# Performance work log

Measured on AMD Instinct MI355X. Metric: run time of the kernel, lower is better.

The kernel has to match this reference:

```python
import jax, jax.numpy as jnp
import numpy as np
from jax import lax


def _conv2d(x, w, b, pad):
    out = lax.conv_general_dilated(x, w, window_strides=(1, 1),
                                   padding=[(pad, pad), (pad, pad)])
    return out + b[None, :, None, None]


def _modulated_deform_conv(x, off_w, off_b, w, b, k, pad):
    """Modulated deformable conv (deformable_groups=1, stride=1, 'same' pad)."""
    B, C, H, W = x.shape
    K2 = k * k
    # offset/mask conv: 3*K2 channels -> (dy, dx, mask_logits)
    om = _conv2d(x, off_w, off_b, pad)              # [B, 3*K2, H, W]
    dy, dx, mlog = om[:, :K2], om[:, K2:2 * K2], om[:, 2 * K2:]
    mask = jax.nn.sigmoid(mlog)                     # [B, K2, H, W]

    xp = jnp.pad(x, ((0, 0), (0, 0), (pad, pad), (pad, pad)))
    Hp, Wp = H + 2 * pad, W + 2 * pad
    Ho, Wo = H, W                                   # stride 1, pad = k//2

    ky, kx = jnp.meshgrid(jnp.arange(k), jnp.arange(k), indexing='ij')
    ky = ky.reshape(1, K2, 1, 1).astype(x.dtype)
    kx = kx.reshape(1, K2, 1, 1).astype(x.dtype)
    iy = jnp.arange(Ho, dtype=x.dtype).reshape(1, 1, Ho, 1)
    ix = jnp.arange(Wo, dtype=x.dtype).reshape(1, 1, 1, Wo)

    py = iy + ky + dy                               # [B, K2, Ho, Wo] sample y (padded coords)
    px = ix + kx + dx                               # [B, K2, Ho, Wo] sample x

    y0f = jnp.floor(py); x0f = jnp.floor(px)
    ty = py - y0f; tx = px - x0f
    y0 = y0f.astype(jnp.int32); x0 = x0f.astype(jnp.int32)
    y1 = y0 + 1; x1 = x0 + 1

    xp_flat = xp.reshape(B, C, Hp * Wp)

    def gather(yi, xi):
        valid = ((yi >= 0) & (yi < Hp) & (xi >= 0) & (xi < Wp)).astype(x.dtype)
        yc = jnp.clip(yi, 0, Hp - 1)
        xc = jnp.clip(xi, 0, Wp - 1)
        idx = (yc * Wp + xc).reshape(B, 1, K2 * Ho * Wo)
        v = jnp.take_along_axis(xp_flat, idx, axis=2).reshape(B, C, K2, Ho, Wo)
        return v * valid[:, None]                   # zero-pad outside

    w00 = ((1 - ty) * (1 - tx))[:, None]
    w01 = ((1 - ty) * tx)[:, None]
    w10 = (ty * (1 - tx))[:, None]
    w11 = (ty * tx)[:, None]

    cols = (gather(y0, x0) * w00 + gather(y0, x1) * w01 +
            gather(y1, x0) * w10 + gather(y1, x1) * w11)
    cols = cols * mask[:, None]                     # [B, C, K2, Ho, Wo]

    O = w.shape[0]
    out = jnp.einsum('bckhw,ock->bohw', cols, w.reshape(O, C, K2))
    return out + b[None, :, None, None]


def setup_inputs() -> dict:
    key = jax.random.key(0)
    ks = jax.random.split(key, 12)
    B, Cin, H, W = 8, 64, 56, 56
    Ch = 128  # out_channels // 2

    def rn(k, shape, scale):
        return jax.random.normal(k, shape, dtype=jnp.float32) * scale

    return {
        'x': rn(ks[0], (B, Cin, H, W), 1.0),
        'w3': rn(ks[1], (Ch, Cin, 3, 3), 0.05),
        'b3': rn(ks[2], (Ch,), 0.05),
        'off3_w': rn(ks[3], (3 * 9, Cin, 3, 3), 0.01),
        'off3_b': rn(ks[4], (3 * 9,), 0.01),
        'w5': rn(ks[5], (Ch, Cin, 5, 5), 0.03),
        'b5': rn(ks[6], (Ch,), 0.05),
        'off5_w': rn(ks[7], (3 * 25, Cin, 5, 5), 0.01),
        'off5_b': rn(ks[8], (3 * 25,), 0.01),
        'sub_w': rn(ks[9], (Ch, Cin, 1, 1), 0.1),
        'sub_b': rn(ks[10], (Ch,), 0.05),
    }


def reference(x, w3, b3, off3_w, off3_b, w5, b5, off5_w, off5_b, sub_w, sub_b):
    x3 = _modulated_deform_conv(x, off3_w, off3_b, w3, b3, k=3, pad=1)
    x5 = _modulated_deform_conv(x, off5_w, off5_b, w5, b5, k=5, pad=2)
    xs = _conv2d(x, sub_w, sub_b, pad=0)            # 1x1 shortcut projection
    x3 = x3 + xs
    x5 = x5 + xs
    out = jnp.concatenate((x3, x5), axis=1)
    return jax.nn.relu(out)
```

## Files before the change

kernel.cpp:

```cpp
#include <hip/hip_runtime.h>
#include <hip/hip_bf16.h>
#include <math.h>

typedef __attribute__((ext_vector_type(8))) short short8;
typedef __attribute__((ext_vector_type(4))) float f32x4;

#define US_XP    0
#define N_XP     (8*60*60*64)
#define US_WOFF  (US_XP + N_XP)
#define N_WOFF   (26*2*8*64*8)
#define US_W5    (US_WOFF + N_WOFF)
#define N_W5     (26*2*8*64*8)
#define US_W3    (US_W5 + N_W5)
#define N_W3     (10*2*8*64*8)
#define US_TOT   (US_W3 + N_W3)
#define FB_BYTES (((US_TOT*2) + 15) & ~15)
#define F_BOM    0
#define F_B5     128
#define F_B3     256
#define N_ITEMS  (8*34*3136)
#define F_OFFS   384
#define F_WTS    (F_OFFS + N_ITEMS*4)

__device__ __forceinline__ unsigned short f2bf(float f) {
    union { float f; unsigned u; } v; v.f = f;
    unsigned r = v.u + 0x7FFFu + ((v.u >> 16) & 1u);
    return (unsigned short)(r >> 16);
}
__device__ __forceinline__ unsigned pack2(float lo, float hi) {
    __hip_bfloat162 h = __float22bfloat162_rn(make_float2(lo, hi));
    return *(unsigned*)&h;
}
__device__ __forceinline__ unsigned blend2(unsigned a, unsigned b, unsigned c, unsigned d,
                                           float w00, float w01, float w10, float w11) {
    float lo = __uint_as_float(a << 16) * w00 + __uint_as_float(b << 16) * w01
             + __uint_as_float(c << 16) * w10 + __uint_as_float(d << 16) * w11;
    float hi = __uint_as_float(a & 0xffff0000u) * w00 + __uint_as_float(b & 0xffff0000u) * w01
             + __uint_as_float(c & 0xffff0000u) * w10 + __uint_as_float(d & 0xffff0000u) * w11;
    return pack2(lo, hi);
}

__global__ __launch_bounds__(256) void xpose(const float* __restrict__ x,
                                             unsigned short* __restrict__ xp)
{
    __shared__ float ld[64*65];
    const int b   = blockIdx.y;
    const int px0 = blockIdx.x * 64;
    const int t   = threadIdx.x;
#pragma unroll
    for (int c0 = 0; c0 < 64; c0 += 4) {
        const int c = c0 + (t >> 6);
        const int p = t & 63;
        ld[c*65 + p] = x[((size_t)(b*64 + c))*3136 + px0 + p];
    }
    __syncthreads();
    const int lp = t >> 2;
    const int ch0 = (t & 3) * 16;
    const int px = px0 + lp;
    const int oy = px/56, ox = px - oy*56;
    unsigned short* dst = xp + ((size_t)b*3600 + (oy+2)*60 + (ox+2))*64 + ch0;
    unsigned short tmp[16];
#pragma unroll
    for (int k = 0; k < 16; ++k) tmp[k] = f2bf(ld[(ch0 + k)*65 + lp]);
    *(uint4*)dst       = *(uint4*)&tmp[0];
    *(uint4*)(dst + 8) = *(uint4*)&tmp[8];
}

__global__ __launch_bounds__(256) void prep_w(
    const float* __restrict__ w3, const float* __restrict__ b3,
    const float* __restrict__ off3w, const float* __restrict__ off3b,
    const float* __restrict__ w5, const float* __restrict__ b5,
    const float* __restrict__ off5w, const float* __restrict__ off5b,
    const float* __restrict__ subw, const float* __restrict__ subb,
    unsigned short* __restrict__ us, float* __restrict__ fb)
{
    const int NTOT = US_TOT + 384;
    for (int i = US_WOFF + blockIdx.x*256 + threadIdx.x; i < NTOT; i += gridDim.x*256) {
        if (i < US_TOT) {
            float v = 0.f;
            int j, mode;
            if (i < US_W5)      { j = i - US_WOFF; mode = 0; }
            else if (i < US_W3) { j = i - US_W5;   mode = 1; }
            else                { j = i - US_W3;   mode = 2; }
            int j8   = j & 7;
            int lane = (j >> 3) & 63;
            int oct  = (j >> 9) & 7;
            int kt   = (j >> 12) & 1;
            int tap  = j >> 13;
            int oc   = oct*16 + (lane & 15);
            int c    = kt*32 + (lane >> 4)*8 + j8;
            if (mode == 0) {
                if (oc < 27 && tap < 25) {
                    int ky = tap/5, kx = tap%5;
                    if (ky>=1 && ky<=3 && kx>=1 && kx<=3)
                        v = off3w[((oc*64 + c)*3 + (ky-1))*3 + (kx-1)];
                } else if (oc >= 27 && oc < 102 && tap < 25) {
                    v = off5w[((oc-27)*64 + c)*25 + tap];
                }
            } else if (mode == 1) {
                v = (tap < 25) ? w5[(oc*64 + c)*25 + tap] : subw[oc*64 + c];
            } else {
                v = (tap < 9) ? w3[(oc*64 + c)*9 + tap] : subw[oc*64 + c];
            }
            us[i] = f2bf(v);
        } else {
            int fj = i - US_TOT;
            float v;
            if (fj < 128)      v = (fj < 27) ? off3b[fj] : ((fj < 102) ? off5b[fj-27] : 0.f);
            else if (fj < 256) { int o = fj-128; v = b5[o] + subb[o]; }
            else               { int o = fj-256; v = b3[o] + subb[o]; }
            fb[fj] = v;
        }
    }
}

__global__ __launch_bounds__(256, 6) void convo3(
    const unsigned short* __restrict__ xp,
    const unsigned short* __restrict__ wp, const float* __restrict__ bias,
    int4* __restrict__ offs, uint2* __restrict__ wts)
{
    const int b    = blockIdx.y;
    const int pix0 = blockIdx.x * 32;
    const int lane = threadIdx.x & 63;
    const int wave = threadIdx.x >> 6;
    const int r15 = lane & 15, q4 = lane >> 4;
    const int cg  = lane & 7,  pr = lane >> 3;

    __shared__ __align__(16) unsigned short cols[2][2][32*72];

    f32x4 acc[2][2] = {{{0.f,0.f,0.f,0.f},{0.f,0.f,0.f,0.f}},
                       {{0.f,0.f,0.f,0.f},{0.f,0.f,0.f,0.f}}};

    const char* xb = (const char*)(xp + (size_t)b*(60*60*64));
    const int px  = wave*8 + pr;
    const int pix = pix0 + px;
    const int oy  = pix/56, ox = pix - oy*56;
    const int coff = (((oy+2)*60) + ox + 2) << 7;

    uint4 G0, G1;
    auto issue = [&](int ta, int tb) {
        int ka = 0, kb = 0;
        if (ta < 25) { int ky = ta/5, kx = ta - ky*5; ka = ((ky-2)*60 + (kx-2)) << 7; }
        if (tb < 25) { int ky = tb/5, kx = tb - ky*5; kb = ((ky-2)*60 + (kx-2)) << 7; }
        G0 = *(const uint4*)(xb + coff + ka + cg*16);
        G1 = *(const uint4*)(xb + coff + kb + cg*16);
    };
    auto commit = [&](unsigned short* bufa, unsigned short* bufb) {
        *(uint4*)&bufa[px*72 + cg*8] = G0;
        *(uint4*)&bufb[px*72 + cg*8] = G1;
    };
    auto gemm = [&](int tap, const unsigned short* buf) {
#pragma unroll
        for (int kt = 0; kt < 2; ++kt) {
            short8 A0 = *(const short8*)(wp + ((size_t)((tap*2+kt)*8 + wave*2    )*64 + lane)*8);
            short8 A1 = *(const short8*)(wp + ((size_t)((tap*2+kt)*8 + wave*2 + 1)*64 + lane)*8);
#pragma unroll
            for (int pt = 0; pt < 2; ++pt) {
                short8 Bf = *(const short8*)(buf + (pt*16 + r15)*72 + kt*32 + q4*8);
                acc[0][pt] = __builtin_amdgcn_mfma_f32_16x16x32_bf16(A0, Bf, acc[0][pt], 0, 0, 0);
                acc[1][pt] = __builtin_amdgcn_mfma_f32_16x16x32_bf16(A1, Bf, acc[1][pt], 0, 0, 0);
            }
        }
    };

    issue(0, 1);
    commit(cols[0][0], cols[0][1]);
    __syncthreads();
    for (int r = 0; r < 13; ++r) {
        if (r + 1 < 13) issue(2*r+2, 2*r+3);
        gemm(2*r,   cols[r&1][0]);
        gemm(2*r+1, cols[r&1][1]);
        if (r + 1 < 13) commit(cols[(r+1)&1][0], cols[(r+1)&1][1]);
        __syncthreads();
    }

    float* omt = (float*)cols;
#pragma unroll
    for (int i = 0; i < 2; ++i)
#pragma unroll
    for (int pt = 0; pt < 2; ++pt)
#pragma unroll
    for (int reg = 0; reg < 4; ++reg) {
        const int oc = (wave*2 + i)*16 + q4*4 + reg;
        const int p2 = pt*16 + r15;
        omt[oc*32 + p2] = acc[i][pt][reg] + bias[oc];
    }
    __syncthreads();

    const int tid = threadIdx.x;
#pragma unroll
    for (int itr = 0; itr < 5; ++itr) {
        const int idx = itr*256 + tid;
        if (idx >= 34*32) break;
        const int t  = idx >> 5;
        const int p2 = idx & 31;
        const int pix2 = pix0 + p2;
        const int oy2 = pix2/56, ox2 = pix2 - oy2*56;
        int ky, kx, cdy, cdx, cml, HP, SH;
        if (t < 25) { ky = t/5; kx = t%5; cdy = 27+t; cdx = 52+t; cml = 77+t; HP = 60; SH = 0; }
        else { int tt = t-25; ky = tt/3; kx = tt%3; cdy = tt; cdx = 9+tt; cml = 18+tt; HP = 58; SH = 1; }
        const float dy = omt[cdy*32 + p2];
        const float dx = omt[cdx*32 + p2];
        const float ml = omt[cml*32 + p2];
        const float mask = 1.f / (1.f + __expf(-ml));
        const float py = (float)(oy2 + ky) + dy;
        const float qx = (float)(ox2 + kx) + dx;
        const float y0f = floorf(py), x0f = floorf(qx);
        const float ty = py - y0f, tx = qx - x0f;
        const int y0 = (int)y0f, x0 = (int)x0f, y1 = y0+1, x1 = x0+1;
        float w00 = (1.f-ty)*(1.f-tx)*mask;
        float w01 = (1.f-ty)*tx*mask;
        float w10 = ty*(1.f-tx)*mask;
        float w11 = ty*tx*mask;
        const bool vy0 = (unsigned)y0 < (unsigned)HP, vy1 = (unsigned)y1 < (unsigned)HP;
        const bool vx0 = (unsigned)x0 < (unsigned)HP, vx1 = (unsigned)x1 < (unsigned)HP;
        if (!(vy0 && vx0)) w00 = 0.f;
        if (!(vy0 && vx1)) w01 = 0.f;
        if (!(vy1 && vx0)) w10 = 0.f;
        if (!(vy1 && vx1)) w11 = 0.f;
        const int yc0 = min(max(y0,0),HP-1)+SH, yc1 = min(max(y1,0),HP-1)+SH;
        const int xc0 = min(max(x0,0),HP-1)+SH, xc1 = min(max(x1,0),HP-1)+SH;
        const int mi = (b*34 + t)*3136 + pix2;
        offs[mi] = make_int4((yc0*60+xc0)<<7, (yc0*60+xc1)<<7, (yc1*60+xc0)<<7, (yc1*60+xc1)<<7);
        wts[mi]  = make_uint2(pack2(w00,w01), pack2(w10,w11));
    }
}

__global__ __launch_bounds__(256, 3) void convd5(
    const unsigned short* __restrict__ xp,
    const int4* __restrict__ offs, const uint2* __restrict__ wts,
    float* __restrict__ out,
    const unsigned short* __restrict__ wp5, const float* __restrict__ bias5,
    const unsigned short* __restrict__ wp3, const float* __restrict__ bias3)
{
    const int kind = blockIdx.z;
    const unsigned short* wp = kind ? wp3 : wp5;
    const float* bias = kind ? bias3 : bias5;
    const int R     = kind ? 5  : 13;
    const int K2    = kind ? 9  : 25;
    const int tofs  = kind ? 25 : 0;
    const int outc0 = kind ? 0  : 128;

    const int b    = blockIdx.y;
    const int pix0 = blockIdx.x * 32;
    const int lane = threadIdx.x & 63;
    const int wave = threadIdx.x >> 6;
    const int r15 = lane & 15, q4 = lane >> 4;
    const int cg  = lane & 7,  pr = lane >> 3;

    __shared__ __align__(16) unsigned short cols[2][2][32*72];

    f32x4 acc[2][2] = {{{0.f,0.f,0.f,0.f},{0.f,0.f,0.f,0.f}},
                       {{0.f,0.f,0.f,0.f},{0.f,0.f,0.f,0.f}}};

    const char* xb = (const char*)(xp + (size_t)b*(60*60*64));
    const int px  = wave*8 + pr;
    const int pix = pix0 + px;
    const int oy  = pix/56, ox = pix - oy*56;
    const int coff  = (((oy+2)*60) + ox + 2) << 7;
    const int mbase = (b*34 + tofs)*3136 + pix;

    uint4 C0[4], C1[4];
    uint2 WC0, WC1;
    int4  MOc0, MOc1, MOn0, MOn1;
    uint2 MWc0, MWc1, MWn0, MWn1;
    short8 Aa[8];

    auto loadMetaN = [&](int ta, int tb) {
        const int a  = min(ta, K2-1) * 3136;
        const int bb = min(tb, K2-1) * 3136;
        MOn0 = offs[mbase + a];  MWn0 = wts[mbase + a];
        MOn1 = offs[mbase + bb]; MWn1 = wts[mbase + bb];
    };
    auto issue = [&](int ta, int tb) {
        if (ta >= K2) {
            C0[0] = *(const uint4*)(xb + coff + cg*16);
        } else {
            WC0 = MWc0;
            C0[0] = *(const uint4*)(xb + MOc0.x + cg*16);
            C0[1] = *(const uint4*)(xb + MOc0.y + cg*16);
            C0[2] = *(const uint4*)(xb + MOc0.z + cg*16);
            C0[3] = *(const uint4*)(xb + MOc0.w + cg*16);
        }
        if (tb >= K2) {
            C1[0] = *(const uint4*)(xb + coff + cg*16);
        } else {
            WC1 = MWc1;
            C1[0] = *(const uint4*)(xb + MOc1.x + cg*16);
            C1[1] = *(const uint4*)(xb + MOc1.y + cg*16);
            C1[2] = *(const uint4*)(xb + MOc1.z + cg*16);
            C1[3] = *(const uint4*)(xb + MOc1.w + cg*16);
        }
    };
    auto commit = [&](int ta, int tb, unsigned short* ba, unsigned short* bb) {
        uint4 res;
        if (ta >= K2) {
            res = C0[0];
        } else {
            const float w00 = __uint_as_float(WC0.x << 16);
            const float w01 = __uint_as_float(WC0.x & 0xffff0000u);
            const float w10 = __uint_as_float(WC0.y << 16);
            const float w11 = __uint_as_float(WC0.y & 0xffff0000u);
            res.x = blend2(C0[0].x, C0[1].x, C0[2].x, C0[3].x, w00, w01, w10, w11);
            res.y = blend2(C0[0].y, C0[1].y, C0[2].y, C0[3].y, w00, w01, w10, w11);
            res.z = blend2(C0[0].z, C0[1].z, C0[2].z, C0[3].z, w00, w01, w10, w11);
            res.w = blend2(C0[0].w, C0[1].w, C0[2].w, C0[3].w, w00, w01, w10, w11);
        }
        *(uint4*)&ba[px*72 + cg*8] = res;
        if (tb >= K2) {
            res = C1[0];
        } else {
            const float w00 = __uint_as_float(WC1.x << 16);
            const float w01 = __uint_as_float(WC1.x & 0xffff0000u);
            const float w10 = __uint_as_float(WC1.y << 16);
            const float w11 = __uint_as_float(WC1.y & 0xffff0000u);
            res.x = blend2(C1[0].x, C1[1].x, C1[2].x, C1[3].x, w00, w01, w10, w11);
            res.y = blend2(C1[0].y, C1[1].y, C1[2].y, C1[3].y, w00, w01, w10, w11);
            res.z = blend2(C1[0].z, C1[1].z, C1[2].z, C1[3].z, w00, w01, w10, w11);
            res.w = blend2(C1[0].w, C1[1].w, C1[2].w, C1[3].w, w00, w01, w10, w11);
        }
        *(uint4*)&bb[px*72 + cg*8] = res;
    };
    auto loadA = [&](int r) {
#pragma unroll
        for (int tt = 0; tt < 2; ++tt)
#pragma unroll
        for (int kt = 0; kt < 2; ++kt)
#pragma unroll
        for (int i = 0; i < 2; ++i)
            Aa[tt*4+kt*2+i] = *(const short8*)(wp + ((size_t)(((2*r+tt)*2+kt)*8 + wave*2 + i)*64 + lane)*8);
    };
    auto gemmT = [&](int tt, const unsigned short* buf) {
#pragma unroll
        for (int kt = 0; kt < 2; ++kt)
#pragma unroll
            for (int pt = 0; pt < 2; ++pt) {
                short8 B = *(const short8*)(buf + (pt*16 + r15)*72 + kt*32 + q4*8);
                acc[0][pt] = __builtin_amdgcn_mfma_f32_16x16x32_bf16(Aa[tt*4+kt*2+0], B, acc[0][pt], 0, 0, 0);
                acc[1][pt] = __builtin_amdgcn_mfma_f32_16x16x32_bf16(Aa[tt*4+kt*2+1], B, acc[1][pt], 0, 0, 0);
            }
    };

    loadMetaN(0, 1);
    MOc0 = MOn0; MWc0 = MWn0; MOc1 = MOn1; MWc1 = MWn1;
    issue(0, 1);
    loadMetaN(2, 3);
    loadA(0);
    commit(0, 1, cols[0][0], cols[0][1]);
    __syncthreads();

    for (int r = 0; r < R; ++r) {
        const bool more = (r + 1 < R);
        if (more) {
            MOc0 = MOn0; MWc0 = MWn0; MOc1 = MOn1; MWc1 = MWn1;
            issue(2*r+2, 2*r+3);
            loadMetaN(2*r+4, 2*r+5);
        }
        gemmT(0, cols[r&1][0]);
        gemmT(1, cols[r&1][1]);
        if (more) {
            loadA(r + 1);
            commit(2*r+2, 2*r+3, cols[(r+1)&1][0], cols[(r+1)&1][1]);
        }
        __syncthreads();
    }

#pragma unroll
    for (int i = 0; i < 2; ++i)
#pragma unroll
    for (int pt = 0; pt < 2; ++pt)
#pragma unroll
    for (int reg = 0; reg < 4; ++reg) {
        const int oc = (wave*2 + i)*16 + q4*4 + reg;
        const int p2 = pix0 + pt*16 + r15;
        float v = fmaxf(acc[i][pt][reg] + bias[oc], 0.f);
        out[((size_t)b*256 + outc0 + oc)*3136 + p2] = v;
    }
}

extern "C" void kernel_launch(void* const* d_in, const int* in_sizes, int n_in,
                              void* d_out, int out_size, void* d_ws, size_t ws_size,
                              hipStream_t stream)
{
    (void)in_sizes; (void)n_in; (void)out_size; (void)ws_size;
    const float* x     = (const float*)d_in[0];
    const float* w3    = (const float*)d_in[1];
    const float* b3    = (const float*)d_in[2];
    const float* off3w = (const float*)d_in[3];
    const float* off3b = (const float*)d_in[4];
    const float* w5    = (const float*)d_in[5];
    const float* b5    = (const float*)d_in[6];
    const float* off5w = (const float*)d_in[7];
    const float* off5b = (const float*)d_in[8];
    const float* subw  = (const float*)d_in[9];
    const float* subb  = (const float*)d_in[10];

    unsigned short* us = (unsigned short*)d_ws;
    float* fb   = (float*)((char*)d_ws + FB_BYTES);
    int4*  offs = (int4*)(fb + F_OFFS);
    uint2* wts  = (uint2*)(fb + F_WTS);
    float* out  = (float*)d_out;

    hipMemsetAsync(us + US_XP, 0, (size_t)N_XP * 2, stream);
    xpose<<<dim3(49, 8), dim3(256), 0, stream>>>(x, us + US_XP);
    prep_w<<<dim3(512), dim3(256), 0, stream>>>(
        w3, b3, off3w, off3b, w5, b5, off5w, off5b, subw, subb, us, fb);

    convo3<<<dim3(98, 8), dim3(256), 0, stream>>>(
        us + US_XP, us + US_WOFF, fb + F_BOM, offs, wts);

    convd5<<<dim3(98, 8, 2), dim3(256), 0, stream>>>(
        us + US_XP, offs, wts, out,
        us + US_W5, fb + F_B5, us + US_W3, fb + F_B3);
}
```

Measured before the change: 156.8 us.

## Switch to fp16 MFMA with packed-half bilinear blend, 4-tap stages, fused border zeroing

Data and weights are now stored as fp16 instead of bf16, and the kernels use f16 MFMA. The deformable bilinear blend runs as packed half2 math instead of unpacking to fp32. Both conv kernels now stage 4 taps per double-buffered round instead of 2, which halves the barrier count but doubles LDS use, and the offset conv's occupancy hint drops from 6 to 4. The full-buffer memset is replaced by an extra xpose block that zeros only the padding border. Together these trade fp16 range and blend precision for less ALU work and fewer launches and syncs.

```diff
diff --git a/kernel.cpp b/kernel.cpp
--- a/kernel.cpp
+++ b/kernel.cpp
@@ -1,18 +1,18 @@
 #include <hip/hip_runtime.h>
-#include <hip/hip_bf16.h>
 #include <math.h>
 
-typedef __attribute__((ext_vector_type(8))) short short8;
+typedef _Float16 half8 __attribute__((ext_vector_type(8)));
+typedef _Float16 half2v __attribute__((ext_vector_type(2)));
 typedef __attribute__((ext_vector_type(4))) float f32x4;
 
 #define US_XP    0
 #define N_XP     (8*60*60*64)
 #define US_WOFF  (US_XP + N_XP)
-#define N_WOFF   (26*2*8*64*8)
+#define N_WOFF   (28*2*8*64*8)
 #define US_W5    (US_WOFF + N_WOFF)
-#define N_W5     (26*2*8*64*8)
+#define N_W5     (28*2*8*64*8)
 #define US_W3    (US_W5 + N_W5)
-#define N_W3     (10*2*8*64*8)
+#define N_W3     (12*2*8*64*8)
 #define US_TOT   (US_W3 + N_W3)
 #define FB_BYTES (((US_TOT*2) + 15) & ~15)
 #define F_BOM    0
@@ -22,29 +22,42 @@
 #define F_OFFS   384
 #define F_WTS    (F_OFFS + N_ITEMS*4)
 
-__device__ __forceinline__ unsigned short f2bf(float f) {
-    union { float f; unsigned u; } v; v.f = f;
-    unsigned r = v.u + 0x7FFFu + ((v.u >> 16) & 1u);
-    return (unsigned short)(r >> 16);
-}
-__device__ __forceinline__ unsigned pack2(float lo, float hi) {
-    __hip_bfloat162 h = __float22bfloat162_rn(make_float2(lo, hi));
-    return *(unsigned*)&h;
-}
-__device__ __forceinline__ unsigned blend2(unsigned a, unsigned b, unsigned c, unsigned d,
-                                           float w00, float w01, float w10, float w11) {
-    float lo = __uint_as_float(a << 16) * w00 + __uint_as_float(b << 16) * w01
-             + __uint_as_float(c << 16) * w10 + __uint_as_float(d << 16) * w11;
-    float hi = __uint_as_float(a & 0xffff0000u) * w00 + __uint_as_float(b & 0xffff0000u) * w01
-             + __uint_as_float(c & 0xffff0000u) * w10 + __uint_as_float(d & 0xffff0000u) * w11;
-    return pack2(lo, hi);
+__device__ __forceinline__ unsigned short f2h(float f) {
+    union { _Float16 h; unsigned short s; } c; c.h = (_Float16)f; return c.s;
+}
+__device__ __forceinline__ half2v splat_lo(unsigned u) {
+    union { unsigned short s; _Float16 h; } c; c.s = (unsigned short)(u & 0xffffu);
+    return (half2v){c.h, c.h};
+}
+__device__ __forceinline__ half2v splat_hi(unsigned u) {
+    union { unsigned short s; _Float16 h; } c; c.s = (unsigned short)(u >> 16);
+    return (half2v){c.h, c.h};
+}
+__device__ __forceinline__ unsigned blendh(unsigned a, unsigned b, unsigned c, unsigned d,
+                                           half2v W00, half2v W01, half2v W10, half2v W11) {
+    union { unsigned u; half2v h; } A, B, C, D, R;
+    A.u = a; B.u = b; C.u = c; D.u = d;
+    R.h = A.h*W00 + B.h*W01 + C.h*W10 + D.h*W11;
+    return R.u;
 }
 
 __global__ __launch_bounds__(256) void xpose(const float* __restrict__ x,
                                              unsigned short* __restrict__ xp)
 {
+    const int b = blockIdx.y;
+    if (blockIdx.x == 49) {
+        const uint4 z = make_uint4(0,0,0,0);
+        for (int i = threadIdx.x; i < 464*8; i += 256) {
+            const int px = i >> 3, part = i & 7;
+            int oy, ox;
+            if (px < 120)      { oy = px/60;            ox = px%60; }
+            else if (px < 240) { int j = px-120; oy = 58 + j/60; ox = j%60; }
+            else               { int j = px-240; oy = 2 + (j>>2); ox = ((j&2)?58:0) + (j&1); }
+            *(uint4*)(xp + ((size_t)b*3600 + oy*60 + ox)*64 + part*8) = z;
+        }
+        return;
+    }
     __shared__ float ld[64*65];
-    const int b   = blockIdx.y;
     const int px0 = blockIdx.x * 64;
     const int t   = threadIdx.x;
 #pragma unroll
@@ -61,7 +74,7 @@
     unsigned short* dst = xp + ((size_t)b*3600 + (oy+2)*60 + (ox+2))*64 + ch0;
     unsigned short tmp[16];
 #pragma unroll
-    for (int k = 0; k < 16; ++k) tmp[k] = f2bf(ld[(ch0 + k)*65 + lp]);
+    for (int k = 0; k < 16; ++k) tmp[k] = f2h(ld[(ch0 + k)*65 + lp]);
     *(uint4*)dst       = *(uint4*)&tmp[0];
     *(uint4*)(dst + 8) = *(uint4*)&tmp[8];
 }
@@ -98,11 +111,13 @@
                     v = off5w[((oc-27)*64 + c)*25 + tap];
                 }
             } else if (mode == 1) {
-                v = (tap < 25) ? w5[(oc*64 + c)*25 + tap] : subw[oc*64 + c];
+                if (tap < 25)       v = w5[(oc*64 + c)*25 + tap];
+                else if (tap == 25) v = subw[oc*64 + c];
             } else {
-                v = (tap < 9) ? w3[(oc*64 + c)*9 + tap] : subw[oc*64 + c];
+                if (tap < 9)        v = w3[(oc*64 + c)*9 + tap];
+                else if (tap == 9)  v = subw[oc*64 + c];
             }
-            us[i] = f2bf(v);
+            us[i] = f2h(v);
         } else {
             int fj = i - US_TOT;
             float v;
@@ -114,7 +129,7 @@
     }
 }
 
-__global__ __launch_bounds__(256, 6) void convo3(
+__global__ __launch_bounds__(256, 4) void convo6(
     const unsigned short* __restrict__ xp,
     const unsigned short* __restrict__ wp, const float* __restrict__ bias,
     int4* __restrict__ offs, uint2* __restrict__ wts)
@@ -126,7 +141,7 @@
     const int r15 = lane & 15, q4 = lane >> 4;
     const int cg  = lane & 7,  pr = lane >> 3;
 
-    __shared__ __align__(16) unsigned short cols[2][2][32*72];
+    __shared__ __align__(16) unsigned short cols[2][4][32*72];
 
     f32x4 acc[2][2] = {{{0.f,0.f,0.f,0.f},{0.f,0.f,0.f,0.f}},
                        {{0.f,0.f,0.f,0.f},{0.f,0.f,0.f,0.f}}};
@@ -137,40 +152,43 @@
     const int oy  = pix/56, ox = pix - oy*56;
     const int coff = (((oy+2)*60) + ox + 2) << 7;
 
-    uint4 G0, G1;
-    auto issue = [&](int ta, int tb) {
-        int ka = 0, kb = 0;
-        if (ta < 25) { int ky = ta/5, kx = ta - ky*5; ka = ((ky-2)*60 + (kx-2)) << 7; }
-        if (tb < 25) { int ky = tb/5, kx = tb - ky*5; kb = ((ky-2)*60 + (kx-2)) << 7; }
-        G0 = *(const uint4*)(xb + coff + ka + cg*16);
-        G1 = *(const uint4*)(xb + coff + kb + cg*16);
-    };
-    auto commit = [&](unsigned short* bufa, unsigned short* bufb) {
-        *(uint4*)&bufa[px*72 + cg*8] = G0;
-        *(uint4*)&bufb[px*72 + cg*8] = G1;
+    uint4 G[4];
+    auto issue = [&](int t0) {
+#pragma unroll
+        for (int j = 0; j < 4; ++j) {
+            const int t = t0 + j;
+            int k = 0;
+            if (t < 25) { int ky = t/5, kx = t - ky*5; k = ((ky-2)*60 + (kx-2)) << 7; }
+            G[j] = *(const uint4*)(xb + coff + k + cg*16);
+        }
+    };
+    auto commit = [&](unsigned short (*buf)[32*72]) {
+#pragma unroll
+        for (int j = 0; j < 4; ++j)
+            *(uint4*)&buf[j][px*72 + cg*8] = G[j];
     };
     auto gemm = [&](int tap, const unsigned short* buf) {
 #pragma unroll
         for (int kt = 0; kt < 2; ++kt) {
-            short8 A0 = *(const short8*)(wp + ((size_t)((tap*2+kt)*8 + wave*2    )*64 + lane)*8);
-            short8 A1 = *(const short8*)(wp + ((size_t)((tap*2+kt)*8 + wave*2 + 1)*64 + lane)*8);
+            half8 A0 = *(const half8*)(wp + ((size_t)((tap*2+kt)*8 + wave*2    )*64 + lane)*8);
+            half8 A1 = *(const half8*)(wp + ((size_t)((tap*2+kt)*8 + wave*2 + 1)*64 + lane)*8);
 #pragma unroll
             for (int pt = 0; pt < 2; ++pt) {
-                short8 Bf = *(const short8*)(buf + (pt*16 + r15)*72 + kt*32 + q4*8);
-                acc[0][pt] = __builtin_amdgcn_mfma_f32_16x16x32_bf16(A0, Bf, acc[0][pt], 0, 0, 0);
-                acc[1][pt] = __builtin_amdgcn_mfma_f32_16x16x32_bf16(A1, Bf, acc[1][pt], 0, 0, 0);
+                half8 Bf = *(const half8*)(buf + (pt*16 + r15)*72 + kt*32 + q4*8);
+                acc[0][pt] = __builtin_amdgcn_mfma_f32_16x16x32_f16(A0, Bf, acc[0][pt], 0, 0, 0);
+                acc[1][pt] = __builtin_amdgcn_mfma_f32_16x16x32_f16(A1, Bf, acc[1][pt], 0, 0, 0);
             }
         }
     };
 
-    issue(0, 1);
-    commit(cols[0][0], cols[0][1]);
+    issue(0);
+    commit(cols[0]);
     __syncthreads();
-    for (int r = 0; r < 13; ++r) {
-        if (r + 1 < 13) issue(2*r+2, 2*r+3);
-        gemm(2*r,   cols[r&1][0]);
-        gemm(2*r+1, cols[r&1][1]);
-        if (r + 1 < 13) commit(cols[(r+1)&1][0], cols[(r+1)&1][1]);
+    for (int r = 0; r < 7; ++r) {
+        if (r + 1 < 7) issue(4*r + 4);
+#pragma unroll
+        for (int tt = 0; tt < 4; ++tt) gemm(4*r + tt, cols[r&1][tt]);
+        if (r + 1 < 7) commit(cols[(r+1)&1]);
         __syncthreads();
     }
 
@@ -222,11 +240,12 @@
         const int xc0 = min(max(x0,0),HP-1)+SH, xc1 = min(max(x1,0),HP-1)+SH;
         const int mi = (b*34 + t)*3136 + pix2;
         offs[mi] = make_int4((yc0*60+xc0)<<7, (yc0*60+xc1)<<7, (yc1*60+xc0)<<7, (yc1*60+xc1)<<7);
-        wts[mi]  = make_uint2(pack2(w00,w01), pack2(w10,w11));
-    }
-}
-
-__global__ __launch_bounds__(256, 3) void convd5(
+        wts[mi]  = make_uint2((unsigned)f2h(w00) | ((unsigned)f2h(w01) << 16),
+                              (unsigned)f2h(w10) | ((unsigned)f2h(w11) << 16));
+    }
+}
+
+__global__ __launch_bounds__(256, 3) void convd6(
     const unsigned short* __restrict__ xp,
     const int4* __restrict__ offs, const uint2* __restrict__ wts,
     float* __restrict__ out,
@@ -236,7 +255,7 @@
     const int kind = blockIdx.z;
     const unsigned short* wp = kind ? wp3 : wp5;
     const float* bias = kind ? bias3 : bias5;
-    const int R     = kind ? 5  : 13;
+    const int R     = kind ? 3  : 7;
     const int K2    = kind ? 9  : 25;
     const int tofs  = kind ? 25 : 0;
     const int outc0 = kind ? 0  : 128;
@@ -248,7 +267,7 @@
     const int r15 = lane & 15, q4 = lane >> 4;
     const int cg  = lane & 7,  pr = lane >> 3;
 
-    __shared__ __align__(16) unsigned short cols[2][2][32*72];
+    __shared__ __align__(16) unsigned short cols[2][4][32*72];
 
     f32x4 acc[2][2] = {{{0.f,0.f,0.f,0.f},{0.f,0.f,0.f,0.f}},
                        {{0.f,0.f,0.f,0.f},{0.f,0.f,0.f,0.f}}};
@@ -260,108 +279,84 @@
     const int coff  = (((oy+2)*60) + ox + 2) << 7;
     const int mbase = (b*34 + tofs)*3136 + pix;
 
-    uint4 C0[4], C1[4];
-    uint2 WC0, WC1;
-    int4  MOc0, MOc1, MOn0, MOn1;
-    uint2 MWc0, MWc1, MWn0, MWn1;
-    short8 Aa[8];
-
-    auto loadMetaN = [&](int ta, int tb) {
-        const int a  = min(ta, K2-1) * 3136;
-        const int bb = min(tb, K2-1) * 3136;
-        MOn0 = offs[mbase + a];  MWn0 = wts[mbase + a];
-        MOn1 = offs[mbase + bb]; MWn1 = wts[mbase + bb];
-    };
-    auto issue = [&](int ta, int tb) {
-        if (ta >= K2) {
-            C0[0] = *(const uint4*)(xb + coff + cg*16);
-        } else {
-            WC0 = MWc0;
-            C0[0] = *(const uint4*)(xb + MOc0.x + cg*16);
-            C0[1] = *(const uint4*)(xb + MOc0.y + cg*16);
-            C0[2] = *(const uint4*)(xb + MOc0.z + cg*16);
-            C0[3] = *(const uint4*)(xb + MOc0.w + cg*16);
-        }
-        if (tb >= K2) {
-            C1[0] = *(const uint4*)(xb + coff + cg*16);
-        } else {
-            WC1 = MWc1;
-            C1[0] = *(const uint4*)(xb + MOc1.x + cg*16);
-            C1[1] = *(const uint4*)(xb + MOc1.y + cg*16);
-            C1[2] = *(const uint4*)(xb + MOc1.z + cg*16);
-            C1[3] = *(const uint4*)(xb + MOc1.w + cg*16);
-        }
-    };
-    auto commit = [&](int ta, int tb, unsigned short* ba, unsigned short* bb) {
-        uint4 res;
-        if (ta >= K2) {
-            res = C0[0];
-        } else {
-            const float w00 = __uint_as_float(WC0.x << 16);
-            const float w01 = __uint_as_float(WC0.x & 0xffff0000u);
-            const float w10 = __uint_as_float(WC0.y << 16);
-            const float w11 = __uint_as_float(WC0.y & 0xffff0000u);
-            res.x = blend2(C0[0].x, C0[1].x, C0[2].x, C0[3].x, w00, w01, w10, w11);
-            res.y = blend2(C0[0].y, C0[1].y, C0[2].y, C0[3].y, w00, w01, w10, w11);
-            res.z = blend2(C0[0].z, C0[1].z, C0[2].z, C0[3].z, w00, w01, w10, w11);
-            res.w = blend2(C0[0].w, C0[1].w, C0[2].w, C0[3].w, w00, w01, w10, w11);
-        }
-        *(uint4*)&ba[px*72 + cg*8] = res;
-        if (tb >= K2) {
-            res = C1[0];
-        } else {
-            const float w00 = __uint_as_float(WC1.x << 16);
-            const float w01 = __uint_as_float(WC1.x & 0xffff0000u);
-            const float w10 = __uint_as_float(WC1.y << 16);
-            const float w11 = __uint_as_float(WC1.y & 0xffff0000u);
-            res.x = blend2(C1[0].x, C1[1].x, C1[2].x, C1[3].x, w00, w01, w10, w11);
-            res.y = blend2(C1[0].y, C1[1].y, C1[2].y, C1[3].y, w00, w01, w10, w11);
-            res.z = blend2(C1[0].z, C1[1].z, C1[2].z, C1[3].z, w00, w01, w10, w11);
-            res.w = blend2(C1[0].w, C1[1].w, C1[2].w, C1[3].w, w00, w01, w10, w11);
-        }
-        *(uint4*)&bb[px*72 + cg*8] = res;
-    };
-    auto loadA = [&](int r) {
-#pragma unroll
-        for (int tt = 0; tt < 2; ++tt)
-#pragma unroll
-        for (int kt = 0; kt < 2; ++kt)
-#pragma unroll
-        for (int i = 0; i < 2; ++i)
-            Aa[tt*4+kt*2+i] = *(const short8*)(wp + ((size_t)(((2*r+tt)*2+kt)*8 + wave*2 + i)*64 + lane)*8);
-    };
-    auto gemmT = [&](int tt, const unsigned short* buf) {
-#pragma unroll
-        for (int kt = 0; kt < 2; ++kt)
+    uint4 C[4][4];
+    uint2 WC[4];
+    int4  MOc[4], MOn[4];
+    uint2 MWc[4], MWn[4];
+
+    auto loadMetaN = [&](int t0) {
+#pragma unroll
+        for (int j = 0; j < 4; ++j) {
+            const int a = min(t0 + j, K2-1) * 3136;
+            MOn[j] = offs[mbase + a]; MWn[j] = wts[mbase + a];
+        }
+    };
+    auto issue = [&](int t0) {
+#pragma unroll
+        for (int j = 0; j < 4; ++j) {
+            const int t = t0 + j;
+            if (t >= K2) {
+                C[j][0] = *(const uint4*)(xb + coff + cg*16);
+            } else {
+                WC[j] = MWc[j];
+                C[j][0] = *(const uint4*)(xb + MOc[j].x + cg*16);
+                C[j][1] = *(const uint4*)(xb + MOc[j].y + cg*16);
+                C[j][2] = *(const uint4*)(xb + MOc[j].z + cg*16);
+                C[j][3] = *(const uint4*)(xb + MOc[j].w + cg*16);
+            }
+        }
+    };
+    auto commit = [&](int t0, unsigned short (*buf)[32*72]) {
+#pragma unroll
+        for (int j = 0; j < 4; ++j) {
+            const int t = t0 + j;
+            uint4 res;
+            if (t >= K2) {
+                res = C[j][0];
+            } else {
+                const half2v W00 = splat_lo(WC[j].x), W01 = splat_hi(WC[j].x);
+                const half2v W10 = splat_lo(WC[j].y), W11 = splat_hi(WC[j].y);
+                res.x = blendh(C[j][0].x, C[j][1].x, C[j][2].x, C[j][3].x, W00, W01, W10, W11);
+                res.y = blendh(C[j][0].y, C[j][1].y, C[j][2].y, C[j][3].y, W00, W01, W10, W11);
+                res.z = blendh(C[j][0].z, C[j][1].z, C[j][2].z, C[j][3].z, W00, W01, W10, W11);
+                res.w = blendh(C[j][0].w, C[j][1].w, C[j][2].w, C[j][3].w, W00, W01, W10, W11);
+            }
+            *(uint4*)&buf[j][px*72 + cg*8] = res;
+        }
+    };
+    auto gemm = [&](int tap, const unsigned short* buf) {
+#pragma unroll
+        for (int kt = 0; kt < 2; ++kt) {
+            half8 A0 = *(const half8*)(wp + ((size_t)((tap*2+kt)*8 + wave*2    )*64 + lane)*8);
+            half8 A1 = *(const half8*)(wp + ((size_t)((tap*2+kt)*8 + wave*2 + 1)*64 + lane)*8);
 #pragma unroll
             for (int pt = 0; pt < 2; ++pt) {
-                short8 B = *(const short8*)(buf + (pt*16 + r15)*72 + kt*32 + q4*8);
-                acc[0][pt] = __builtin_amdgcn_mfma_f32_16x16x32_bf16(Aa[tt*4+kt*2+0], B, acc[0][pt], 0, 0, 0);
-                acc[1][pt] = __builtin_amdgcn_mfma_f32_16x16x32_bf16(Aa[tt*4+kt*2+1], B, acc[1][pt], 0, 0, 0);
+                half8 B = *(const half8*)(buf + (pt*16 + r15)*72 + kt*32 + q4*8);
+                acc[0][pt] = __builtin_amdgcn_mfma_f32_16x16x32_f16(A0, B, acc[0][pt], 0, 0, 0);
+                acc[1][pt] = __builtin_amdgcn_mfma_f32_16x16x32_f16(A1, B, acc[1][pt], 0, 0, 0);
             }
-    };
-
-    loadMetaN(0, 1);
-    MOc0 = MOn0; MWc0 = MWn0; MOc1 = MOn1; MWc1 = MWn1;
-    issue(0, 1);
-    loadMetaN(2, 3);
-    loadA(0);
-    commit(0, 1, cols[0][0], cols[0][1]);
+        }
+    };
+
+    loadMetaN(0);
+#pragma unroll
+    for (int j = 0; j < 4; ++j) { MOc[j] = MOn[j]; MWc[j] = MWn[j]; }
+    issue(0);
+    loadMetaN(4);
+    commit(0, cols[0]);
     __syncthreads();
 
     for (int r = 0; r < R; ++r) {
         const bool more = (r + 1 < R);
         if (more) {
-            MOc0 = MOn0; MWc0 = MWn0; MOc1 = MOn1; MWc1 = MWn1;
-            issue(2*r+2, 2*r+3);
-            loadMetaN(2*r+4, 2*r+5);
-        }
-        gemmT(0, cols[r&1][0]);
-        gemmT(1, cols[r&1][1]);
-        if (more) {
-            loadA(r + 1);
-            commit(2*r+2, 2*r+3, cols[(r+1)&1][0], cols[(r+1)&1][1]);
-        }
+#pragma unroll
+            for (int j = 0; j < 4; ++j) { MOc[j] = MOn[j]; MWc[j] = MWn[j]; }
+            issue(4*r + 4);
+            loadMetaN(4*r + 8);
+        }
+#pragma unroll
+        for (int tt = 0; tt < 4; ++tt) gemm(4*r + tt, cols[r&1][tt]);
+        if (more) commit(4*r + 4, cols[(r+1)&1]);
         __syncthreads();
     }
 
@@ -401,15 +396,14 @@
     uint2* wts  = (uint2*)(fb + F_WTS);
     float* out  = (float*)d_out;
 
-    hipMemsetAsync(us + US_XP, 0, (size_t)N_XP * 2, stream);
-    xpose<<<dim3(49, 8), dim3(256), 0, stream>>>(x, us + US_XP);
+    xpose<<<dim3(50, 8), dim3(256), 0, stream>>>(x, us + US_XP);
     prep_w<<<dim3(512), dim3(256), 0, stream>>>(
         w3, b3, off3w, off3b, w5, b5, off5w, off5b, subw, subb, us, fb);
 
-    convo3<<<dim3(98, 8), dim3(256), 0, stream>>>(
+    convo6<<<dim3(98, 8), dim3(256), 0, stream>>>(
         us + US_XP, us + US_WOFF, fb + F_BOM, offs, wts);
 
-    convd5<<<dim3(98, 8, 2), dim3(256), 0, stream>>>(
+    convd6<<<dim3(98, 8, 2), dim3(256), 0, stream>>>(
         us + US_XP, offs, wts, out,
         us + US_W5, fb + F_B5, us + US_W3, fb + F_B3);
 }
```

After: 302.7 us. 1.93x slower.
